# Kernel tuning notes

Hardware: AMD Instinct MI355X
Metric: run time of the kernel (lower is better)

The kernel has to match this reference:

```python
import jax, jax.numpy as jnp
import numpy as np


def setup_inputs() -> dict:
    key = jax.random.key(0)
    ks = jax.random.split(key, 7)
    B, T, H, V = 64, 2048, 256, 256
    s = 0.05  # small init scale so tanh/sigmoid stay in a sane range
    return {
        "x": jax.random.randint(ks[0], (B, T), 0, V, dtype=jnp.int64),
        "W_ih": jax.random.normal(ks[1], (4 * H, V), dtype=jnp.float32) * s,
        "W_hh": jax.random.normal(ks[2], (4 * H, H), dtype=jnp.float32) * s,
        "b_ih": jax.random.normal(ks[3], (4 * H,), dtype=jnp.float32) * s,
        "b_hh": jax.random.normal(ks[4], (4 * H,), dtype=jnp.float32) * s,
        "fc_W": jax.random.normal(ks[5], (V, H), dtype=jnp.float32) * s,
        "fc_b": jax.random.normal(ks[6], (V,), dtype=jnp.float32) * s,
    }


def reference(x, W_ih, W_hh, b_ih, b_hh, fc_W, fc_b):
    # one_hot(x) @ W_ih.T  ==  gather rows of W_ih.T by token id (same math, no
    # [B,T,256] one-hot tensor materialized)
    B, T = x.shape
    H = W_hh.shape[1]
    x_proj = W_ih.T[x] + b_ih  # [B, T, 4H] input contributions, precomputed once

    def step(carry, xt):
        h, c = carry
        gates = xt + h @ W_hh.T + b_hh  # [B, 4H]; PyTorch gate order i,f,g,o
        i, f, g, o = jnp.split(gates, 4, axis=-1)
        i = jax.nn.sigmoid(i)
        f = jax.nn.sigmoid(f)
        g = jnp.tanh(g)
        o = jax.nn.sigmoid(o)
        c = f * c + i * g
        h = o * jnp.tanh(c)
        return (h, c), h

    h0 = jnp.zeros((B, H), dtype=x_proj.dtype)
    c0 = jnp.zeros((B, H), dtype=x_proj.dtype)
    (hT, cT), hs = jax.lax.scan(step, (h0, c0), jnp.swapaxes(x_proj, 0, 1))
    out = jnp.swapaxes(hs, 0, 1)  # [B, T, H] (batch_first)
    logits = out @ fc_W.T + fc_b  # [B, T, 256]
    return logits, hT[None], cT[None]  # h_n, c_n have shape [1, B, H]
```

## Files before the change

### kernel.cpp

```cpp
#include <hip/hip_runtime.h>
#include <stdint.h>

#define TT 2048
#define BB 64
#define HH 256

#define WIHT_OFF 0
#define BIAS_OFF 262144
#define HBUF_OFF 263168
#define XMAP_OFF 328704
#define WS_TOT   328960

#define LOGITS   33554432

__global__ __launch_bounds__(256, 1) void k_prep(const float* __restrict__ W_ih,
                                                 const float* __restrict__ b_ih,
                                                 const float* __restrict__ b_hh,
                                                 float* ws_f) {
    int idx = blockIdx.x * 256 + threadIdx.x;
    if (idx < 262144) {
        int v = idx >> 10, r = idx & 1023;
        ws_f[WIHT_OFF + idx] = W_ih[r * 256 + v];
    } else if (idx < 263168) {
        int r = idx - 262144;
        ws_f[idx] = b_ih[r] + b_hh[r];
    } else if (idx < WS_TOT) {
        ws_f[idx] = 0.0f;
    }
}

__device__ __forceinline__ float sigm_f(float x) { return 1.0f / (1.0f + __expf(-x)); }
__device__ __forceinline__ float tanh_f(float x) {
    float e = __expf(2.0f * x);
    return 1.0f - 2.0f / (e + 1.0f);
}

__device__ __forceinline__ unsigned long long ld_l2(const unsigned long long* p) {
    unsigned long long v;
    asm volatile("global_load_dwordx2 %0, %1, off sc0\n\ts_waitcnt vmcnt(0)"
                 : "=v"(v) : "v"(p) : "memory");
    return v;
}

__global__ __launch_bounds__(256, 1) void k_lstm(const int* __restrict__ x,
                                                 const float* __restrict__ W_hh,
                                                 float* ws_f,
                                                 float* out) {
    const int tid = threadIdx.x;
    const int bid = blockIdx.x;
    const int xcd  = bid & 7;
    const int slot = bid >> 3;
    const int b = xcd + 8 * (slot >> 2);
    const int q = slot & 3;
    const int u  = tid & 63;
    const int w  = tid >> 6;
    const int gt = w;
    const int j  = q * 64 + u;
    const int r  = gt * 256 + j;

    __shared__ alignas(16) float hin[192];
    __shared__ alignas(16) float hloc[64];
    __shared__ float gbuf[256];
    __shared__ int xs[4];

    float4 w4[64];
#pragma unroll
    for (int i = 0; i < 64; ++i) {
        int cb = (i < 48) ? ((q + 1 + (i >> 4)) & 3) : q;
        int wi = (i < 48) ? (i & 15) : (i - 48);
        w4[i] = *(const float4*)(W_hh + (size_t)r * 256 + cb * 64 + wi * 4);
    }
    const float bias_r = ws_f[BIAS_OFF + r];
    unsigned long long* hbuf = (unsigned long long*)(ws_f + HBUF_OFF);
    unsigned* xmap = (unsigned*)ws_f + XMAP_OFF;
    const int* xrow = x + b * TT;
    const bool ownw = (w == q);
    const int rb = (w - q + 3) & 3;

    int myxcc = 0;
    asm volatile("s_getreg_b32 %0, hwreg(HW_REG_XCC_ID)" : "=s"(myxcc));
    if (tid == 0)
        __hip_atomic_store(&xmap[bid], 0x100u | (unsigned)myxcc,
                           __ATOMIC_RELAXED, __HIP_MEMORY_SCOPE_AGENT);
    if (tid < 4) {
        int pb = (b & 7) + 8 * ((b >> 3) * 4 + tid);
        unsigned v; int g = 0;
        do {
            v = __hip_atomic_load(&xmap[pb], __ATOMIC_RELAXED, __HIP_MEMORY_SCOPE_AGENT);
        } while (!(v & 0x100u) && ++g < (1 << 20));
        xs[tid] = (v & 0x100u) ? (int)(v & 0xffu) : -1 - tid;
    }
    if (tid < 64) hloc[tid] = 0.0f;
    float c_state = 0.0f;
    __syncthreads();
    bool fastm = (xs[0] == xs[1]) & (xs[1] == xs[2]) & (xs[2] == xs[3]);

    const float4* hin4 = (const float4*)hin;
    const float4* hl4  = (const float4*)hloc;

    for (int t = 0; t < TT; ++t) {
        const int p = t & 1;
        int tok = xrow[t];
        float xw = ws_f[WIHT_OFF + tok * 1024 + r] + bias_r;

        float a0 = 0.f, a1 = 0.f, a2 = 0.f, a3 = 0.f;
#pragma unroll
        for (int i = 0; i < 16; ++i) {
            float4 hh = hl4[i];
            a0 += w4[48 + i].x * hh.x;
            a1 += w4[48 + i].y * hh.y;
            a2 += w4[48 + i].z * hh.z;
            a3 += w4[48 + i].w * hh.w;
        }

        if (!ownw) {
            const unsigned long long* src = hbuf + (size_t)p * (BB * HH) + b * HH + tid;
            const unsigned ut = (unsigned)t;
            unsigned long long v = 0;
            if (fastm) {
                int g = 0;
                do { v = ld_l2(src); } while ((unsigned)(v >> 32) != ut && ++g < 6000);
                if ((unsigned)(v >> 32) != ut) fastm = false;
            }
            if (!fastm) {
                int g = 0;
                do {
                    v = __hip_atomic_load(src, __ATOMIC_RELAXED, __HIP_MEMORY_SCOPE_AGENT);
                } while ((unsigned)(v >> 32) != ut && ++g < (1 << 21));
            }
            hin[rb * 64 + u] = __uint_as_float((unsigned)v);
        }
        __syncthreads();

#pragma unroll
        for (int i = 0; i < 48; ++i) {
            float4 hh = hin4[i];
            a0 += w4[i].x * hh.x;
            a1 += w4[i].y * hh.y;
            a2 += w4[i].z * hh.z;
            a3 += w4[i].w * hh.w;
        }
        float gate = xw + ((a0 + a1) + (a2 + a3));
        float act = (gt == 2) ? tanh_f(gate) : sigm_f(gate);
        gbuf[tid] = act;
        __syncthreads();

        if (tid < 64) {
            float ig = gbuf[tid], fg = gbuf[64 + tid];
            float gg = gbuf[128 + tid], og = gbuf[192 + tid];
            c_state = fg * c_state + ig * gg;
            float hval = og * tanh_f(c_state);
            unsigned long long pv =
                ((unsigned long long)(unsigned)(t + 1) << 32) |
                (unsigned long long)__float_as_uint(hval);
            __hip_atomic_store(hbuf + (size_t)((t + 1) & 1) * (BB * HH) + b * HH + j,
                               pv, __ATOMIC_RELAXED, __HIP_MEMORY_SCOPE_AGENT);
            hloc[tid] = hval;
            out[((size_t)(b * TT + t) << 8) + j] = hval;
            if (t == TT - 1) {
                out[LOGITS + b * HH + j] = hval;
                out[LOGITS + BB * HH + b * HH + j] = c_state;
            }
        }
        __syncthreads();
    }
}

__global__ __launch_bounds__(256, 1) void k_fc(const float* __restrict__ fc_W,
                                               const float* __restrict__ fc_b,
                                               float* out) {
    __shared__ alignas(16) float ht[64][256];
    const int tid = threadIdx.x;
    const size_t base = (size_t)blockIdx.x * 64;
    for (int i = 0; i < 64; ++i)
        ht[i][tid] = out[(base + i) * 256 + tid];

    float4 w4[64];
    const float4* wr = (const float4*)(fc_W + (size_t)tid * 256);
#pragma unroll
    for (int k = 0; k < 64; ++k) w4[k] = wr[k];
    const float bias = fc_b[tid];
    __syncthreads();

    for (int m = 0; m < 64; ++m) {
        const float4* hv = (const float4*)ht[m];
        float a0 = 0.f, a1 = 0.f, a2 = 0.f, a3 = 0.f;
#pragma unroll
        for (int k = 0; k < 64; ++k) {
            float4 hh = hv[k];
            a0 += w4[k].x * hh.x;
            a1 += w4[k].y * hh.y;
            a2 += w4[k].z * hh.z;
            a3 += w4[k].w * hh.w;
        }
        out[(base + m) * 256 + tid] = bias + ((a0 + a1) + (a2 + a3));
    }
}

extern "C" void kernel_launch(void* const* d_in, const int* in_sizes, int n_in,
                              void* d_out, int out_size, void* d_ws, size_t ws_size,
                              hipStream_t stream) {
    const int*   x    = (const int*)d_in[0];
    const float* W_ih = (const float*)d_in[1];
    const float* W_hh = (const float*)d_in[2];
    const float* b_ih = (const float*)d_in[3];
    const float* b_hh = (const float*)d_in[4];
    const float* fc_W = (const float*)d_in[5];
    const float* fc_b = (const float*)d_in[6];
    float* out  = (float*)d_out;
    float* ws_f = (float*)d_ws;

    k_prep<<<(WS_TOT + 255) / 256, 256, 0, stream>>>(W_ih, b_ih, b_hh, ws_f);
    k_lstm<<<256, 256, 0, stream>>>(x, W_hh, ws_f, out);
    k_fc<<<2048, 256, 0, stream>>>(fc_W, fc_b, out);
}
```

Baseline: 6.355 ms.

## Fuse FC projection into LSTM loop and interleave gates per thread with shuffles

Each thread now handles one gate of one hidden unit, with the four gates for a unit held in adjacent lanes. The gate values are combined through warp shuffles, which removes the gbuf shared-memory round trip and one __syncthreads per step. The separate k_fc kernel is removed: each step computes the previous timestep's logits from the already-gathered h vector, using per-thread fc_W slices held in registers, and writes them with nontemporal stores. The next token's input projection is prefetched one step ahead and h buffers are double-buffered in LDS. The cost is extra register pressure from fc_W and extra FC work inside the serial recurrence loop.

```diff
diff --git a/kernel.cpp b/kernel.cpp
--- a/kernel.cpp
+++ b/kernel.cpp
@@ -29,7 +29,6 @@
     }
 }
 
-__device__ __forceinline__ float sigm_f(float x) { return 1.0f / (1.0f + __expf(-x)); }
 __device__ __forceinline__ float tanh_f(float x) {
     float e = __expf(2.0f * x);
     return 1.0f - 2.0f / (e + 1.0f);
@@ -44,23 +43,27 @@
 
 __global__ __launch_bounds__(256, 1) void k_lstm(const int* __restrict__ x,
                                                  const float* __restrict__ W_hh,
-                                                 float* ws_f,
-                                                 float* out) {
+                                                 const float* __restrict__ wsro,
+                                                 unsigned long long* __restrict__ hbuf,
+                                                 unsigned* __restrict__ xmap,
+                                                 const float* __restrict__ fc_W,
+                                                 const float* __restrict__ fc_b,
+                                                 float* __restrict__ out) {
     const int tid = threadIdx.x;
     const int bid = blockIdx.x;
     const int xcd  = bid & 7;
     const int slot = bid >> 3;
     const int b = xcd + 8 * (slot >> 2);
     const int q = slot & 3;
+    const int w  = tid >> 6;
     const int u  = tid & 63;
-    const int w  = tid >> 6;
-    const int gt = w;
-    const int j  = q * 64 + u;
-    const int r  = gt * 256 + j;
-
-    __shared__ alignas(16) float hin[192];
-    __shared__ alignas(16) float hloc[64];
-    __shared__ float gbuf[256];
+    const int s  = tid & 3;
+    const int uj = tid >> 2;
+    const int jg = q * 64 + uj;
+    const int r  = s * 256 + jg;
+
+    __shared__ alignas(16) float hin[2][192];
+    __shared__ alignas(16) float hloc[2][64];
     __shared__ int xs[4];
 
     float4 w4[64];
@@ -70,12 +73,13 @@
         int wi = (i < 48) ? (i & 15) : (i - 48);
         w4[i] = *(const float4*)(W_hh + (size_t)r * 256 + cb * 64 + wi * 4);
     }
-    const float bias_r = ws_f[BIAS_OFF + r];
-    unsigned long long* hbuf = (unsigned long long*)(ws_f + HBUF_OFF);
-    unsigned* xmap = (unsigned*)ws_f + XMAP_OFF;
+    float4 fw[16];
+#pragma unroll
+    for (int i = 0; i < 16; ++i)
+        fw[i] = *(const float4*)(fc_W + (size_t)jg * 256 + s * 64 + i * 4);
+    const float bias_r = wsro[BIAS_OFF + r];
+    const float fcb = fc_b[jg];
     const int* xrow = x + b * TT;
-    const bool ownw = (w == q);
-    const int rb = (w - q + 3) & 3;
 
     int myxcc = 0;
     asm volatile("s_getreg_b32 %0, hwreg(HW_REG_XCC_ID)" : "=s"(myxcc));
@@ -90,31 +94,24 @@
         } while (!(v & 0x100u) && ++g < (1 << 20));
         xs[tid] = (v & 0x100u) ? (int)(v & 0xffu) : -1 - tid;
     }
-    if (tid < 64) hloc[tid] = 0.0f;
+    if (tid < 64) hloc[0][tid] = 0.0f;
     float c_state = 0.0f;
     __syncthreads();
     bool fastm = (xs[0] == xs[1]) & (xs[1] == xs[2]) & (xs[2] == xs[3]);
 
-    const float4* hin4 = (const float4*)hin;
-    const float4* hl4  = (const float4*)hloc;
+    const bool pollme = (tid < 192);
+    const int cq = (q + 1 + w) & 3;
+
+    float xw_cur = wsro[WIHT_OFF + xrow[0] * 1024 + r] + bias_r;
+    float hval = 0.0f;
 
     for (int t = 0; t < TT; ++t) {
-        const int p = t & 1;
-        int tok = xrow[t];
-        float xw = ws_f[WIHT_OFF + tok * 1024 + r] + bias_r;
-
-        float a0 = 0.f, a1 = 0.f, a2 = 0.f, a3 = 0.f;
-#pragma unroll
-        for (int i = 0; i < 16; ++i) {
-            float4 hh = hl4[i];
-            a0 += w4[48 + i].x * hh.x;
-            a1 += w4[48 + i].y * hh.y;
-            a2 += w4[48 + i].z * hh.z;
-            a3 += w4[48 + i].w * hh.w;
-        }
-
-        if (!ownw) {
-            const unsigned long long* src = hbuf + (size_t)p * (BB * HH) + b * HH + tid;
+        const int tn = (t + 1 < TT) ? t + 1 : t;
+        const float xw_next_raw = wsro[WIHT_OFF + xrow[tn] * 1024 + r];
+
+        if (pollme) {
+            const unsigned long long* src =
+                hbuf + (size_t)(t & 1) * (BB * HH) + b * HH + cq * 64 + u;
             const unsigned ut = (unsigned)t;
             unsigned long long v = 0;
             if (fastm) {
@@ -128,72 +125,114 @@
                     v = __hip_atomic_load(src, __ATOMIC_RELAXED, __HIP_MEMORY_SCOPE_AGENT);
                 } while ((unsigned)(v >> 32) != ut && ++g < (1 << 21));
             }
-            hin[rb * 64 + u] = __uint_as_float((unsigned)v);
+            hin[t & 1][w * 64 + u] = __uint_as_float((unsigned)v);
         }
         __syncthreads();
 
+        const float4* hl4 = (const float4*)hloc[t & 1];
+        const float4* hn4 = (const float4*)hin[t & 1];
+        float a0 = 0.f, a1 = 0.f, a2 = 0.f, a3 = 0.f;
+#pragma unroll
+        for (int i = 0; i < 16; ++i) {
+            float4 hh = hl4[i];
+            a0 += w4[48 + i].x * hh.x;
+            a1 += w4[48 + i].y * hh.y;
+            a2 += w4[48 + i].z * hh.z;
+            a3 += w4[48 + i].w * hh.w;
+        }
 #pragma unroll
         for (int i = 0; i < 48; ++i) {
-            float4 hh = hin4[i];
+            float4 hh = hn4[i];
             a0 += w4[i].x * hh.x;
             a1 += w4[i].y * hh.y;
             a2 += w4[i].z * hh.z;
             a3 += w4[i].w * hh.w;
         }
-        float gate = xw + ((a0 + a1) + (a2 + a3));
-        float act = (gt == 2) ? tanh_f(gate) : sigm_f(gate);
-        gbuf[tid] = act;
-        __syncthreads();
-
-        if (tid < 64) {
-            float ig = gbuf[tid], fg = gbuf[64 + tid];
-            float gg = gbuf[128 + tid], og = gbuf[192 + tid];
-            c_state = fg * c_state + ig * gg;
-            float hval = og * tanh_f(c_state);
+        float gate = xw_cur + ((a0 + a1) + (a2 + a3));
+        const float B2 = (s == 2) ? 2.0f : 1.0f;
+        float ex = __expf(B2 * gate);
+        float act = 1.0f - B2 / (ex + 1.0f);
+
+        const int qb = u & ~3;
+        float ig = __shfl(act, qb + 0);
+        float fg = __shfl(act, qb + 1);
+        float gg = __shfl(act, qb + 2);
+        float og = __shfl(act, qb + 3);
+        c_state = fg * c_state + ig * gg;
+        hval = og * tanh_f(c_state);
+
+        if (s == 0) {
             unsigned long long pv =
                 ((unsigned long long)(unsigned)(t + 1) << 32) |
                 (unsigned long long)__float_as_uint(hval);
-            __hip_atomic_store(hbuf + (size_t)((t + 1) & 1) * (BB * HH) + b * HH + j,
+            __hip_atomic_store(hbuf + (size_t)((t + 1) & 1) * (BB * HH) + b * HH + jg,
                                pv, __ATOMIC_RELAXED, __HIP_MEMORY_SCOPE_AGENT);
-            hloc[tid] = hval;
-            out[((size_t)(b * TT + t) << 8) + j] = hval;
-            if (t == TT - 1) {
-                out[LOGITS + b * HH + j] = hval;
-                out[LOGITS + BB * HH + b * HH + j] = c_state;
+            hloc[(t + 1) & 1][uj] = hval;
+        }
+
+        if (t > 0) {
+            const float4* hs = (s == q) ? hl4 : (hn4 + ((s - q + 3) & 3) * 16);
+            float b0 = 0.f, b1 = 0.f, b2 = 0.f, b3 = 0.f;
+#pragma unroll
+            for (int k = 0; k < 16; ++k) {
+                float4 hh = hs[k];
+                b0 += fw[k].x * hh.x;
+                b1 += fw[k].y * hh.y;
+                b2 += fw[k].z * hh.z;
+                b3 += fw[k].w * hh.w;
             }
-        }
-        __syncthreads();
-    }
-}
-
-__global__ __launch_bounds__(256, 1) void k_fc(const float* __restrict__ fc_W,
-                                               const float* __restrict__ fc_b,
-                                               float* out) {
-    __shared__ alignas(16) float ht[64][256];
-    const int tid = threadIdx.x;
-    const size_t base = (size_t)blockIdx.x * 64;
-    for (int i = 0; i < 64; ++i)
-        ht[i][tid] = out[(base + i) * 256 + tid];
-
-    float4 w4[64];
-    const float4* wr = (const float4*)(fc_W + (size_t)tid * 256);
-#pragma unroll
-    for (int k = 0; k < 64; ++k) w4[k] = wr[k];
-    const float bias = fc_b[tid];
+            float lg = (b0 + b1) + (b2 + b3);
+            lg += __shfl_xor(lg, 1);
+            lg += __shfl_xor(lg, 2);
+            if (s == 0)
+                __builtin_nontemporal_store(lg + fcb,
+                    out + ((size_t)(b * TT + (t - 1)) << 8) + jg);
+        }
+        xw_cur = xw_next_raw + bias_r;
+    }
+
+    if (s == 0) {
+        __builtin_nontemporal_store(hval,    out + LOGITS + b * HH + jg);
+        __builtin_nontemporal_store(c_state, out + LOGITS + BB * HH + b * HH + jg);
+    }
+
+    if (pollme) {
+        const unsigned long long* src = hbuf + b * HH + cq * 64 + u;
+        const unsigned ut = (unsigned)TT;
+        unsigned long long v = 0;
+        if (fastm) {
+            int g = 0;
+            do { v = ld_l2(src); } while ((unsigned)(v >> 32) != ut && ++g < 6000);
+            if ((unsigned)(v >> 32) != ut) fastm = false;
+        }
+        if (!fastm) {
+            int g = 0;
+            do {
+                v = __hip_atomic_load(src, __ATOMIC_RELAXED, __HIP_MEMORY_SCOPE_AGENT);
+            } while ((unsigned)(v >> 32) != ut && ++g < (1 << 21));
+        }
+        hin[0][w * 64 + u] = __uint_as_float((unsigned)v);
+    }
     __syncthreads();
-
-    for (int m = 0; m < 64; ++m) {
-        const float4* hv = (const float4*)ht[m];
-        float a0 = 0.f, a1 = 0.f, a2 = 0.f, a3 = 0.f;
-#pragma unroll
-        for (int k = 0; k < 64; ++k) {
-            float4 hh = hv[k];
-            a0 += w4[k].x * hh.x;
-            a1 += w4[k].y * hh.y;
-            a2 += w4[k].z * hh.z;
-            a3 += w4[k].w * hh.w;
-        }
-        out[(base + m) * 256 + tid] = bias + ((a0 + a1) + (a2 + a3));
+    {
+        const float4* hl4 = (const float4*)hloc[0];
+        const float4* hn4 = (const float4*)hin[0];
+        const float4* hs = (s == q) ? hl4 : (hn4 + ((s - q + 3) & 3) * 16);
+        float b0 = 0.f, b1 = 0.f, b2 = 0.f, b3 = 0.f;
+#pragma unroll
+        for (int k = 0; k < 16; ++k) {
+            float4 hh = hs[k];
+            b0 += fw[k].x * hh.x;
+            b1 += fw[k].y * hh.y;
+            b2 += fw[k].z * hh.z;
+            b3 += fw[k].w * hh.w;
+        }
+        float lg = (b0 + b1) + (b2 + b3);
+        lg += __shfl_xor(lg, 1);
+        lg += __shfl_xor(lg, 2);
+        if (s == 0)
+            __builtin_nontemporal_store(lg + fcb,
+                out + ((size_t)(b * TT + (TT - 1)) << 8) + jg);
     }
 }
 
@@ -209,8 +248,9 @@
     const float* fc_b = (const float*)d_in[6];
     float* out  = (float*)d_out;
     float* ws_f = (float*)d_ws;
+    unsigned long long* hbuf = (unsigned long long*)(ws_f + HBUF_OFF);
+    unsigned* xmap = (unsigned*)(ws_f + XMAP_OFF);
 
     k_prep<<<(WS_TOT + 255) / 256, 256, 0, stream>>>(W_ih, b_ih, b_hh, ws_f);
-    k_lstm<<<256, 256, 0, stream>>>(x, W_hh, ws_f, out);
-    k_fc<<<2048, 256, 0, stream>>>(fc_W, fc_b, out);
-}
+    k_lstm<<<256, 256, 0, stream>>>(x, W_hh, ws_f, hbuf, xmap, fc_W, fc_b, out);
+}
```

Result: slower. 8.833 ms (+39.0%).

## Remove per-step barrier via double-buffered LDS and redundant cell updates

Applied to the files above, without the earlier changes.

Every wave now does the cell-state update itself, so the third __syncthreads per timestep goes away. To keep this safe, the hin and gbuf LDS buffers are double-buffered and hloc is replicated once per wave. The next step's input projection is prefetched one iteration ahead. Only the owning wave publishes h, with an extra sc0 store when the fast path is on. The risk is the added redundant activation math and the doubled global store on the hot path.

```diff
diff --git a/kernel.cpp b/kernel.cpp
--- a/kernel.cpp
+++ b/kernel.cpp
@@ -41,11 +41,16 @@
                  : "=v"(v) : "v"(p) : "memory");
     return v;
 }
+__device__ __forceinline__ void st_l2(unsigned long long* p, unsigned long long v) {
+    asm volatile("global_store_dwordx2 %0, %1, off sc0" :: "v"(p), "v"(v) : "memory");
+}
 
 __global__ __launch_bounds__(256, 1) void k_lstm(const int* __restrict__ x,
                                                  const float* __restrict__ W_hh,
-                                                 float* ws_f,
-                                                 float* out) {
+                                                 const float* __restrict__ wsro,
+                                                 unsigned long long* __restrict__ hbuf,
+                                                 unsigned* __restrict__ xmap,
+                                                 float* __restrict__ out) {
     const int tid = threadIdx.x;
     const int bid = blockIdx.x;
     const int xcd  = bid & 7;
@@ -54,13 +59,12 @@
     const int q = slot & 3;
     const int u  = tid & 63;
     const int w  = tid >> 6;
-    const int gt = w;
     const int j  = q * 64 + u;
-    const int r  = gt * 256 + j;
-
-    __shared__ alignas(16) float hin[192];
-    __shared__ alignas(16) float hloc[64];
-    __shared__ float gbuf[256];
+    const int r  = w * 256 + j;
+
+    __shared__ alignas(16) float hin[2][192];
+    __shared__ alignas(16) float hloc[4][64];
+    __shared__ float gbuf[2][256];
     __shared__ int xs[4];
 
     float4 w4[64];
@@ -70,9 +74,7 @@
         int wi = (i < 48) ? (i & 15) : (i - 48);
         w4[i] = *(const float4*)(W_hh + (size_t)r * 256 + cb * 64 + wi * 4);
     }
-    const float bias_r = ws_f[BIAS_OFF + r];
-    unsigned long long* hbuf = (unsigned long long*)(ws_f + HBUF_OFF);
-    unsigned* xmap = (unsigned*)ws_f + XMAP_OFF;
+    const float bias_r = wsro[BIAS_OFF + r];
     const int* xrow = x + b * TT;
     const bool ownw = (w == q);
     const int rb = (w - q + 3) & 3;
@@ -90,18 +92,20 @@
         } while (!(v & 0x100u) && ++g < (1 << 20));
         xs[tid] = (v & 0x100u) ? (int)(v & 0xffu) : -1 - tid;
     }
-    if (tid < 64) hloc[tid] = 0.0f;
+    hloc[w][u] = 0.0f;
     float c_state = 0.0f;
+    float hval = 0.0f;
     __syncthreads();
     bool fastm = (xs[0] == xs[1]) & (xs[1] == xs[2]) & (xs[2] == xs[3]);
 
-    const float4* hin4 = (const float4*)hin;
-    const float4* hl4  = (const float4*)hloc;
+    const float4* hl4 = (const float4*)hloc[w];
+
+    float xw_cur = wsro[WIHT_OFF + xrow[0] * 1024 + r] + bias_r;
 
     for (int t = 0; t < TT; ++t) {
         const int p = t & 1;
-        int tok = xrow[t];
-        float xw = ws_f[WIHT_OFF + tok * 1024 + r] + bias_r;
+        const int tn = (t + 1 < TT) ? t + 1 : t;
+        const float xw_next_raw = wsro[WIHT_OFF + xrow[tn] * 1024 + r];
 
         float a0 = 0.f, a1 = 0.f, a2 = 0.f, a3 = 0.f;
 #pragma unroll
@@ -128,41 +132,46 @@
                     v = __hip_atomic_load(src, __ATOMIC_RELAXED, __HIP_MEMORY_SCOPE_AGENT);
                 } while ((unsigned)(v >> 32) != ut && ++g < (1 << 21));
             }
-            hin[rb * 64 + u] = __uint_as_float((unsigned)v);
+            hin[p][rb * 64 + u] = __uint_as_float((unsigned)v);
         }
         __syncthreads();
 
+        const float4* hn4 = (const float4*)hin[p];
 #pragma unroll
         for (int i = 0; i < 48; ++i) {
-            float4 hh = hin4[i];
+            float4 hh = hn4[i];
             a0 += w4[i].x * hh.x;
             a1 += w4[i].y * hh.y;
             a2 += w4[i].z * hh.z;
             a3 += w4[i].w * hh.w;
         }
-        float gate = xw + ((a0 + a1) + (a2 + a3));
-        float act = (gt == 2) ? tanh_f(gate) : sigm_f(gate);
-        gbuf[tid] = act;
+        float gate = xw_cur + ((a0 + a1) + (a2 + a3));
+        float act = (w == 2) ? tanh_f(gate) : sigm_f(gate);
+        gbuf[p][tid] = act;
         __syncthreads();
 
-        if (tid < 64) {
-            float ig = gbuf[tid], fg = gbuf[64 + tid];
-            float gg = gbuf[128 + tid], og = gbuf[192 + tid];
-            c_state = fg * c_state + ig * gg;
-            float hval = og * tanh_f(c_state);
+        float ig = gbuf[p][u],       fg = gbuf[p][64 + u];
+        float gg = gbuf[p][128 + u], og = gbuf[p][192 + u];
+        c_state = fg * c_state + ig * gg;
+        hval = og * tanh_f(c_state);
+
+        if (ownw) {
             unsigned long long pv =
                 ((unsigned long long)(unsigned)(t + 1) << 32) |
                 (unsigned long long)__float_as_uint(hval);
-            __hip_atomic_store(hbuf + (size_t)((t + 1) & 1) * (BB * HH) + b * HH + j,
-                               pv, __ATOMIC_RELAXED, __HIP_MEMORY_SCOPE_AGENT);
-            hloc[tid] = hval;
+            unsigned long long* dst =
+                hbuf + (size_t)((t + 1) & 1) * (BB * HH) + b * HH + j;
+            if (fastm) st_l2(dst, pv);
+            __hip_atomic_store(dst, pv, __ATOMIC_RELAXED, __HIP_MEMORY_SCOPE_AGENT);
             out[((size_t)(b * TT + t) << 8) + j] = hval;
-            if (t == TT - 1) {
-                out[LOGITS + b * HH + j] = hval;
-                out[LOGITS + BB * HH + b * HH + j] = c_state;
-            }
-        }
-        __syncthreads();
+        }
+        hloc[w][u] = hval;
+        xw_cur = xw_next_raw + bias_r;
+    }
+
+    if (ownw) {
+        out[LOGITS + b * HH + j] = hval;
+        out[LOGITS + BB * HH + b * HH + j] = c_state;
     }
 }
 
@@ -209,8 +218,10 @@
     const float* fc_b = (const float*)d_in[6];
     float* out  = (float*)d_out;
     float* ws_f = (float*)d_ws;
+    unsigned long long* hbuf = (unsigned long long*)(ws_f + HBUF_OFF);
+    unsigned* xmap = (unsigned*)(ws_f + XMAP_OFF);
 
     k_prep<<<(WS_TOT + 255) / 256, 256, 0, stream>>>(W_ih, b_ih, b_hh, ws_f);
-    k_lstm<<<256, 256, 0, stream>>>(x, W_hh, ws_f, out);
+    k_lstm<<<256, 256, 0, stream>>>(x, W_hh, ws_f, hbuf, xmap, out);
     k_fc<<<2048, 256, 0, stream>>>(fc_W, fc_b, out);
 }
```

Result: faster. 6.200 ms (-2.4%).
